# Kernel tuning notes

Hardware: AMD Instinct MI355X
Metric: run time of the kernel (lower is better)

The kernel has to match this reference:

```python
import jax, jax.numpy as jnp
import numpy as np

NUM_BLOCKS = 256
BLOCK_SIZE = 256
BATCH = 16
MAX_BLOCKS = 8            # max_context_len = MAX_BLOCKS * BLOCK_SIZE = 2048
NUM_HEADS = 32
NUM_KV_HEADS = 8
HEAD_DIM = 128
SCALE = 1.0 / np.sqrt(HEAD_DIM).astype(np.float32)


def setup_inputs() -> dict:
    key = jax.random.key(0)
    ks = jax.random.split(key, 5)
    q = jax.random.normal(ks[0], (BATCH, NUM_HEADS, HEAD_DIM), dtype=jnp.float32)
    k = jax.random.normal(ks[1], (BATCH, NUM_KV_HEADS, HEAD_DIM), dtype=jnp.float32)
    v = jax.random.normal(ks[2], (BATCH, NUM_KV_HEADS, HEAD_DIM), dtype=jnp.float32)
    k_cache = jax.random.normal(ks[3], (NUM_BLOCKS, BLOCK_SIZE, NUM_KV_HEADS, HEAD_DIM), dtype=jnp.float32)
    v_cache = jax.random.normal(ks[4], (NUM_BLOCKS, BLOCK_SIZE, NUM_KV_HEADS, HEAD_DIM), dtype=jnp.float32)
    rng = np.random.default_rng(0)
    # distinct blocks per sequence (16*8 = 128 <= 256 available blocks)
    block_tables = rng.permutation(NUM_BLOCKS)[: BATCH * MAX_BLOCKS].reshape(BATCH, MAX_BLOCKS).astype(np.int32)
    context_lens = rng.integers(1, MAX_BLOCKS * BLOCK_SIZE + 1, size=(BATCH,)).astype(np.int32)
    pos = context_lens - 1  # slot of the token being written this decode step
    slot_mapping = (block_tables[np.arange(BATCH), pos // BLOCK_SIZE] * BLOCK_SIZE + pos % BLOCK_SIZE).astype(np.int32)
    return {
        "q": q, "k": k, "v": v,
        "k_cache": k_cache, "v_cache": v_cache,
        "block_tables": jnp.asarray(block_tables),
        "context_lens": jnp.asarray(context_lens),
        "slot_mapping": jnp.asarray(slot_mapping),
    }


def _store_kv(key_t, value_t, kc_flat, vc_flat, slot_mapping):
    # scatter new K/V tokens to cache slots; slot < 0 means skip
    valid = slot_mapping >= 0
    safe = jnp.where(valid, slot_mapping, 0)
    kc_flat = kc_flat.at[safe].set(jnp.where(valid[:, None, None], key_t, kc_flat[safe]))
    vc_flat = vc_flat.at[safe].set(jnp.where(valid[:, None, None], value_t, vc_flat[safe]))
    return kc_flat, vc_flat


def reference(q, k, v, k_cache, v_cache, block_tables, context_lens, slot_mapping):
    # 1) store current-step K/V to paged cache (flattened view)
    kc_flat = k_cache.reshape(-1, NUM_KV_HEADS, HEAD_DIM)
    vc_flat = v_cache.reshape(-1, NUM_KV_HEADS, HEAD_DIM)
    kc_flat, vc_flat = _store_kv(k, v, kc_flat, vc_flat, slot_mapping)
    kc = kc_flat.reshape(NUM_BLOCKS, BLOCK_SIZE, NUM_KV_HEADS, HEAD_DIM)
    vc = vc_flat.reshape(NUM_BLOCKS, BLOCK_SIZE, NUM_KV_HEADS, HEAD_DIM)

    # 2) gather K/V blocks per sequence -> [B, L, KV, D], L = MAX_BLOCKS*BLOCK_SIZE
    safe_bt = jnp.clip(block_tables, 0, NUM_BLOCKS - 1)
    L = MAX_BLOCKS * BLOCK_SIZE
    k_g = kc[safe_bt.reshape(-1)].reshape(BATCH, L, NUM_KV_HEADS, HEAD_DIM)
    v_g = vc[safe_bt.reshape(-1)].reshape(BATCH, L, NUM_KV_HEADS, HEAD_DIM)
    kv_mask = jnp.arange(L)[None, :] < context_lens[:, None]  # [B, L]

    # 3) grouped-query attention, one query token per sequence
    G = NUM_HEADS // NUM_KV_HEADS
    q_g = q.reshape(BATCH, NUM_KV_HEADS, G, HEAD_DIM)
    scores = jnp.einsum('bkgd,blkd->bkgl', q_g, k_g) * SCALE  # [B, KV, G, L]
    scores = jnp.where(kv_mask[:, None, None, :], scores, -1e9)
    w = jax.nn.softmax(scores, axis=-1)
    out = jnp.einsum('bkgl,blkd->bkgd', w, v_g)
    return out.reshape(BATCH, NUM_HEADS, HEAD_DIM)
```

## Files before the change

kernel.cpp:

```cpp
#include <hip/hip_runtime.h>

#define BATCH 16
#define NUM_HEADS 32
#define NUM_KV 8
#define GQ 4
#define HD 128
#define PAGE 256
#define MAXB 8
#define NS 8
#define TPS 256
#define QSCALE 0.08838834764831845f

#define WS_STRIDE 520

__global__ __launch_bounds__(256) void pa_partial(
    const float* __restrict__ q,
    const float* __restrict__ knew,
    const float* __restrict__ vnew,
    const float* __restrict__ kc,
    const float* __restrict__ vc,
    const int* __restrict__ block_tables,
    const int* __restrict__ context_lens,
    float* __restrict__ ws)
{
  int blk = blockIdx.x;
  int t = blk >> 8;
  int r = blk & 255;
  int b = (t << 2) | (r & 3);
  int kvh = (r >> 2) & 7;
  int split = ((r >> 5) + (t << 1)) & 7;

  int ctx = context_lens[b];
  int start = split * TPS;
  if (start >= ctx) return;
  int n = min(TPS, ctx - start);
  int page = block_tables[b * MAXB + split];
  int pbase = page * PAGE;

  int tid = threadIdx.x;
  int w = tid >> 6;
  int lane = tid & 63;
  int grp = lane >> 4;
  int j = lane & 15;
  int tb = w * 4 + grp;

  __shared__ float4 s_pv[TPS];
  __shared__ float s_redM[4][GQ];
  __shared__ float s_redL[4][GQ];
  __shared__ float s_acc[4][GQ][HD];

  float qr[GQ][8];
  #pragma unroll
  for (int g = 0; g < GQ; ++g) {
    const float* qp = q + ((size_t)(b * NUM_HEADS + kvh * GQ + g)) * HD;
    float4 a = *(const float4*)(qp + j * 4);
    float4 c = *(const float4*)(qp + 64 + j * 4);
    qr[g][0]=a.x*QSCALE; qr[g][1]=a.y*QSCALE; qr[g][2]=a.z*QSCALE; qr[g][3]=a.w*QSCALE;
    qr[g][4]=c.x*QSCALE; qr[g][5]=c.y*QSCALE; qr[g][6]=c.z*QSCALE; qr[g][7]=c.w*QSCALE;
  }

  const float* knew_row = knew + (size_t)(b * NUM_KV + kvh) * HD + j * 4;
  const float* vnew_row = vnew + (size_t)(b * NUM_KV + kvh) * HD + j * 4;
  size_t base_off = ((size_t)pbase * NUM_KV + kvh) * HD + j * 4;
  const float* kbase = kc + base_off;
  const float* vbase = vc + base_off;
  int newpos = ctx - 1 - start;

  int iters = (n + 15) >> 4;

  #pragma unroll 2
  for (int i = 0; i < iters; ++i) {
    int tl = tb + i * 16;
    int tlc = (tl < n) ? tl : 0;
    const float* krow = (tlc == newpos) ? knew_row
                                        : kbase + (size_t)tlc * (NUM_KV * HD);
    float4 k0 = *(const float4*)(krow);
    float4 k1 = *(const float4*)(krow + 64);
    float kk[8] = {k0.x,k0.y,k0.z,k0.w,k1.x,k1.y,k1.z,k1.w};
    float s0 = 0.f, s1 = 0.f, s2 = 0.f, s3 = 0.f;
    #pragma unroll
    for (int e = 0; e < 8; ++e) {
      s0 += qr[0][e] * kk[e];
      s1 += qr[1][e] * kk[e];
      s2 += qr[2][e] * kk[e];
      s3 += qr[3][e] * kk[e];
    }
    #pragma unroll
    for (int mask = 1; mask <= 8; mask <<= 1) {
      s0 += __shfl_xor(s0, mask);
      s1 += __shfl_xor(s1, mask);
      s2 += __shfl_xor(s2, mask);
      s3 += __shfl_xor(s3, mask);
    }
    if (j < 4) {
      float val = (j == 0) ? s0 : (j == 1) ? s1 : (j == 2) ? s2 : s3;
      ((float*)&s_pv[tl])[j] = val;
    }
  }
  __syncthreads();

  float4 sc = s_pv[tid];
  bool valid = tid < n;
  float sv0 = valid ? sc.x : -1e30f;
  float sv1 = valid ? sc.y : -1e30f;
  float sv2 = valid ? sc.z : -1e30f;
  float sv3 = valid ? sc.w : -1e30f;
  float m0 = sv0, m1 = sv1, m2 = sv2, m3 = sv3;
  #pragma unroll
  for (int mask = 1; mask <= 32; mask <<= 1) {
    m0 = fmaxf(m0, __shfl_xor(m0, mask));
    m1 = fmaxf(m1, __shfl_xor(m1, mask));
    m2 = fmaxf(m2, __shfl_xor(m2, mask));
    m3 = fmaxf(m3, __shfl_xor(m3, mask));
  }
  if (lane == 0) {
    s_redM[w][0] = m0; s_redM[w][1] = m1; s_redM[w][2] = m2; s_redM[w][3] = m3;
  }
  __syncthreads();
  float Mg[GQ];
  #pragma unroll
  for (int g = 0; g < GQ; ++g)
    Mg[g] = fmaxf(fmaxf(s_redM[0][g], s_redM[1][g]), fmaxf(s_redM[2][g], s_redM[3][g]));
  float4 p4;
  p4.x = __expf(sv0 - Mg[0]);
  p4.y = __expf(sv1 - Mg[1]);
  p4.z = __expf(sv2 - Mg[2]);
  p4.w = __expf(sv3 - Mg[3]);
  s_pv[tid] = p4;
  float l0 = p4.x, l1 = p4.y, l2 = p4.z, l3 = p4.w;
  #pragma unroll
  for (int mask = 1; mask <= 32; mask <<= 1) {
    l0 += __shfl_xor(l0, mask);
    l1 += __shfl_xor(l1, mask);
    l2 += __shfl_xor(l2, mask);
    l3 += __shfl_xor(l3, mask);
  }
  if (lane == 0) {
    s_redL[w][0] = l0; s_redL[w][1] = l1; s_redL[w][2] = l2; s_redL[w][3] = l3;
  }
  __syncthreads();
  float Lg[GQ];
  #pragma unroll
  for (int g = 0; g < GQ; ++g)
    Lg[g] = s_redL[0][g] + s_redL[1][g] + s_redL[2][g] + s_redL[3][g];

  float acc[GQ][8];
  #pragma unroll
  for (int g = 0; g < GQ; ++g)
    #pragma unroll
    for (int e = 0; e < 8; ++e) acc[g][e] = 0.f;

  #pragma unroll 2
  for (int i = 0; i < iters; ++i) {
    int tl = tb + i * 16;
    int tlc = (tl < n) ? tl : 0;
    const float* vrow = (tlc == newpos) ? vnew_row
                                        : vbase + (size_t)tlc * (NUM_KV * HD);
    float4 v0 = *(const float4*)(vrow);
    float4 v1 = *(const float4*)(vrow + 64);
    float vv[8] = {v0.x,v0.y,v0.z,v0.w,v1.x,v1.y,v1.z,v1.w};
    float4 pp = s_pv[tl];
    #pragma unroll
    for (int e = 0; e < 8; ++e) {
      acc[0][e] += pp.x * vv[e];
      acc[1][e] += pp.y * vv[e];
      acc[2][e] += pp.z * vv[e];
      acc[3][e] += pp.w * vv[e];
    }
  }

  #pragma unroll
  for (int g = 0; g < GQ; ++g)
    #pragma unroll
    for (int e = 0; e < 8; ++e) {
      acc[g][e] += __shfl_xor(acc[g][e], 16);
      acc[g][e] += __shfl_xor(acc[g][e], 32);
    }
  if (lane < 16) {
    #pragma unroll
    for (int g = 0; g < GQ; ++g) {
      #pragma unroll
      for (int e = 0; e < 4; ++e) s_acc[w][g][j * 4 + e] = acc[g][e];
      #pragma unroll
      for (int e = 4; e < 8; ++e) s_acc[w][g][64 + j * 4 + e - 4] = acc[g][e];
    }
  }
  __syncthreads();

  float* outp = ws + (size_t)(((b * NUM_KV) + kvh) * NS + split) * WS_STRIDE;
  #pragma unroll
  for (int idx = tid; idx < GQ * HD; idx += 256) {
    int g = idx >> 7;
    int d = idx & 127;
    float A = s_acc[0][g][d] + s_acc[1][g][d] + s_acc[2][g][d] + s_acc[3][g][d];
    outp[8 + idx] = A;
    if (d == 0) {
      outp[g] = Mg[g];
      outp[GQ + g] = Lg[g];
    }
  }
}

__global__ __launch_bounds__(128) void pa_reduce(
    const float* __restrict__ ws,
    const int* __restrict__ context_lens,
    float* __restrict__ out)
{
  int blk = blockIdx.x;
  int g  = blk & 3;
  int kv = (blk >> 2) & 7;
  int b  = blk >> 5;
  int d  = threadIdx.x;
  int ctx = context_lens[b];
  int ns = (ctx + TPS - 1) / TPS;
  const float* base = ws + (size_t)((b * NUM_KV + kv) * NS) * WS_STRIDE;

  float M = -1e30f;
  for (int s = 0; s < ns; ++s) M = fmaxf(M, base[s * WS_STRIDE + g]);
  float Lsum = 0.f, A = 0.f;
  for (int s = 0; s < ns; ++s) {
    float e = __expf(base[s * WS_STRIDE + g] - M);
    Lsum += base[s * WS_STRIDE + GQ + g] * e;
    A    += base[s * WS_STRIDE + 8 + g * HD + d] * e;
  }
  out[((size_t)(b * NUM_HEADS) + kv * GQ + g) * HD + d] = A / Lsum;
}

extern "C" void kernel_launch(void* const* d_in, const int* in_sizes, int n_in,
                              void* d_out, int out_size, void* d_ws, size_t ws_size,
                              hipStream_t stream) {
  const float* q  = (const float*)d_in[0];
  const float* k  = (const float*)d_in[1];
  const float* v  = (const float*)d_in[2];
  const float* kc = (const float*)d_in[3];
  const float* vc = (const float*)d_in[4];
  const int* block_tables = (const int*)d_in[5];
  const int* context_lens = (const int*)d_in[6];

  float* ws = (float*)d_ws;
  float* out = (float*)d_out;

  pa_partial<<<BATCH * NUM_KV * NS, 256, 0, stream>>>(
      q, k, v, kc, vc, block_tables, context_lens, ws);
  pa_reduce<<<BATCH * NUM_KV * GQ, 128, 0, stream>>>(ws, context_lens, out);
}
```

Baseline: 39.59 us.

## Use persistent work-stealing blocks with finer 128-token splits for paged attention

Replaces the fixed one-block-per-(batch, kv head, split) grid with 1024 persistent blocks that claim work items through a global atomic counter, which is reset each call with a memset. When the workspace is large enough it halves the split size to 128 tokens (16 splits), giving finer load balancing across sequences of uneven context length. The cost is an extra memset launch, an atomic plus a barrier per item, and more partials for the reduce kernel to combine. With 128-token splits, half the threads sit idle in the softmax phase.

```diff
diff --git a/kernel.cpp b/kernel.cpp
--- a/kernel.cpp
+++ b/kernel.cpp
@@ -7,13 +7,14 @@
 #define HD 128
 #define PAGE 256
 #define MAXB 8
-#define NS 8
-#define TPS 256
+#define NGROUP (BATCH * NUM_KV)
 #define QSCALE 0.08838834764831845f
 
 #define WS_STRIDE 520
-
-__global__ __launch_bounds__(256) void pa_partial(
+#define PART_OFF 128
+
+template <int NSPLIT, int TPSZ>
+__global__ __launch_bounds__(256) void pa_partial_steal(
     const float* __restrict__ q,
     const float* __restrict__ knew,
     const float* __restrict__ vnew,
@@ -23,197 +24,223 @@
     const int* __restrict__ context_lens,
     float* __restrict__ ws)
 {
-  int blk = blockIdx.x;
-  int t = blk >> 8;
-  int r = blk & 255;
-  int b = (t << 2) | (r & 3);
-  int kvh = (r >> 2) & 7;
-  int split = ((r >> 5) + (t << 1)) & 7;
-
-  int ctx = context_lens[b];
-  int start = split * TPS;
-  if (start >= ctx) return;
-  int n = min(TPS, ctx - start);
-  int page = block_tables[b * MAXB + split];
-  int pbase = page * PAGE;
+  constexpr int NITEM = NGROUP * NSPLIT;
+  int* cnt = (int*)ws;
+  float* part = ws + PART_OFF;
 
   int tid = threadIdx.x;
   int w = tid >> 6;
   int lane = tid & 63;
-  int grp = lane >> 4;
+  int grp16 = lane >> 4;
   int j = lane & 15;
-  int tb = w * 4 + grp;
-
-  __shared__ float4 s_pv[TPS];
+  int tb = w * 4 + grp16;
+
+  __shared__ float4 s_pv[TPSZ];
   __shared__ float s_redM[4][GQ];
   __shared__ float s_redL[4][GQ];
   __shared__ float s_acc[4][GQ][HD];
-
-  float qr[GQ][8];
-  #pragma unroll
-  for (int g = 0; g < GQ; ++g) {
-    const float* qp = q + ((size_t)(b * NUM_HEADS + kvh * GQ + g)) * HD;
-    float4 a = *(const float4*)(qp + j * 4);
-    float4 c = *(const float4*)(qp + 64 + j * 4);
-    qr[g][0]=a.x*QSCALE; qr[g][1]=a.y*QSCALE; qr[g][2]=a.z*QSCALE; qr[g][3]=a.w*QSCALE;
-    qr[g][4]=c.x*QSCALE; qr[g][5]=c.y*QSCALE; qr[g][6]=c.z*QSCALE; qr[g][7]=c.w*QSCALE;
-  }
-
-  const float* knew_row = knew + (size_t)(b * NUM_KV + kvh) * HD + j * 4;
-  const float* vnew_row = vnew + (size_t)(b * NUM_KV + kvh) * HD + j * 4;
-  size_t base_off = ((size_t)pbase * NUM_KV + kvh) * HD + j * 4;
-  const float* kbase = kc + base_off;
-  const float* vbase = vc + base_off;
-  int newpos = ctx - 1 - start;
-
-  int iters = (n + 15) >> 4;
-
-  #pragma unroll 2
-  for (int i = 0; i < iters; ++i) {
-    int tl = tb + i * 16;
-    int tlc = (tl < n) ? tl : 0;
-    const float* krow = (tlc == newpos) ? knew_row
-                                        : kbase + (size_t)tlc * (NUM_KV * HD);
-    float4 k0 = *(const float4*)(krow);
-    float4 k1 = *(const float4*)(krow + 64);
-    float kk[8] = {k0.x,k0.y,k0.z,k0.w,k1.x,k1.y,k1.z,k1.w};
-    float s0 = 0.f, s1 = 0.f, s2 = 0.f, s3 = 0.f;
-    #pragma unroll
-    for (int e = 0; e < 8; ++e) {
-      s0 += qr[0][e] * kk[e];
-      s1 += qr[1][e] * kk[e];
-      s2 += qr[2][e] * kk[e];
-      s3 += qr[3][e] * kk[e];
-    }
-    #pragma unroll
-    for (int mask = 1; mask <= 8; mask <<= 1) {
-      s0 += __shfl_xor(s0, mask);
-      s1 += __shfl_xor(s1, mask);
-      s2 += __shfl_xor(s2, mask);
-      s3 += __shfl_xor(s3, mask);
-    }
-    if (j < 4) {
-      float val = (j == 0) ? s0 : (j == 1) ? s1 : (j == 2) ? s2 : s3;
-      ((float*)&s_pv[tl])[j] = val;
-    }
-  }
-  __syncthreads();
-
-  float4 sc = s_pv[tid];
-  bool valid = tid < n;
-  float sv0 = valid ? sc.x : -1e30f;
-  float sv1 = valid ? sc.y : -1e30f;
-  float sv2 = valid ? sc.z : -1e30f;
-  float sv3 = valid ? sc.w : -1e30f;
-  float m0 = sv0, m1 = sv1, m2 = sv2, m3 = sv3;
-  #pragma unroll
-  for (int mask = 1; mask <= 32; mask <<= 1) {
-    m0 = fmaxf(m0, __shfl_xor(m0, mask));
-    m1 = fmaxf(m1, __shfl_xor(m1, mask));
-    m2 = fmaxf(m2, __shfl_xor(m2, mask));
-    m3 = fmaxf(m3, __shfl_xor(m3, mask));
-  }
-  if (lane == 0) {
-    s_redM[w][0] = m0; s_redM[w][1] = m1; s_redM[w][2] = m2; s_redM[w][3] = m3;
-  }
-  __syncthreads();
-  float Mg[GQ];
-  #pragma unroll
-  for (int g = 0; g < GQ; ++g)
-    Mg[g] = fmaxf(fmaxf(s_redM[0][g], s_redM[1][g]), fmaxf(s_redM[2][g], s_redM[3][g]));
-  float4 p4;
-  p4.x = __expf(sv0 - Mg[0]);
-  p4.y = __expf(sv1 - Mg[1]);
-  p4.z = __expf(sv2 - Mg[2]);
-  p4.w = __expf(sv3 - Mg[3]);
-  s_pv[tid] = p4;
-  float l0 = p4.x, l1 = p4.y, l2 = p4.z, l3 = p4.w;
-  #pragma unroll
-  for (int mask = 1; mask <= 32; mask <<= 1) {
-    l0 += __shfl_xor(l0, mask);
-    l1 += __shfl_xor(l1, mask);
-    l2 += __shfl_xor(l2, mask);
-    l3 += __shfl_xor(l3, mask);
-  }
-  if (lane == 0) {
-    s_redL[w][0] = l0; s_redL[w][1] = l1; s_redL[w][2] = l2; s_redL[w][3] = l3;
-  }
-  __syncthreads();
-  float Lg[GQ];
-  #pragma unroll
-  for (int g = 0; g < GQ; ++g)
-    Lg[g] = s_redL[0][g] + s_redL[1][g] + s_redL[2][g] + s_redL[3][g];
-
-  float acc[GQ][8];
-  #pragma unroll
-  for (int g = 0; g < GQ; ++g)
-    #pragma unroll
-    for (int e = 0; e < 8; ++e) acc[g][e] = 0.f;
-
-  #pragma unroll 2
-  for (int i = 0; i < iters; ++i) {
-    int tl = tb + i * 16;
-    int tlc = (tl < n) ? tl : 0;
-    const float* vrow = (tlc == newpos) ? vnew_row
-                                        : vbase + (size_t)tlc * (NUM_KV * HD);
-    float4 v0 = *(const float4*)(vrow);
-    float4 v1 = *(const float4*)(vrow + 64);
-    float vv[8] = {v0.x,v0.y,v0.z,v0.w,v1.x,v1.y,v1.z,v1.w};
-    float4 pp = s_pv[tl];
-    #pragma unroll
-    for (int e = 0; e < 8; ++e) {
-      acc[0][e] += pp.x * vv[e];
-      acc[1][e] += pp.y * vv[e];
-      acc[2][e] += pp.z * vv[e];
-      acc[3][e] += pp.w * vv[e];
-    }
-  }
-
-  #pragma unroll
-  for (int g = 0; g < GQ; ++g)
-    #pragma unroll
-    for (int e = 0; e < 8; ++e) {
-      acc[g][e] += __shfl_xor(acc[g][e], 16);
-      acc[g][e] += __shfl_xor(acc[g][e], 32);
-    }
-  if (lane < 16) {
+  __shared__ int s_item;
+
+  for (;;) {
+    if (tid == 0) s_item = atomicAdd(cnt, 1);
+    __syncthreads();
+    int item = s_item;
+    if (item >= NITEM) return;
+
+    int kvh = item & 7;
+    int b = (item >> 3) & 15;
+    int split = item >> 7;
+    int ctx = context_lens[b];
+    int start = split * TPSZ;
+    if (start >= ctx) continue;
+    int n = min(TPSZ, ctx - start);
+    int page = block_tables[b * MAXB + (start >> 8)];
+    int pbase = page * PAGE + (start & (PAGE - 1));
+
+    float qr[GQ][8];
     #pragma unroll
     for (int g = 0; g < GQ; ++g) {
-      #pragma unroll
-      for (int e = 0; e < 4; ++e) s_acc[w][g][j * 4 + e] = acc[g][e];
-      #pragma unroll
-      for (int e = 4; e < 8; ++e) s_acc[w][g][64 + j * 4 + e - 4] = acc[g][e];
-    }
-  }
-  __syncthreads();
-
-  float* outp = ws + (size_t)(((b * NUM_KV) + kvh) * NS + split) * WS_STRIDE;
-  #pragma unroll
-  for (int idx = tid; idx < GQ * HD; idx += 256) {
-    int g = idx >> 7;
-    int d = idx & 127;
-    float A = s_acc[0][g][d] + s_acc[1][g][d] + s_acc[2][g][d] + s_acc[3][g][d];
-    outp[8 + idx] = A;
-    if (d == 0) {
-      outp[g] = Mg[g];
-      outp[GQ + g] = Lg[g];
+      const float* qp = q + ((size_t)(b * NUM_HEADS + kvh * GQ + g)) * HD;
+      float4 a = *(const float4*)(qp + j * 4);
+      float4 c = *(const float4*)(qp + 64 + j * 4);
+      qr[g][0]=a.x*QSCALE; qr[g][1]=a.y*QSCALE; qr[g][2]=a.z*QSCALE; qr[g][3]=a.w*QSCALE;
+      qr[g][4]=c.x*QSCALE; qr[g][5]=c.y*QSCALE; qr[g][6]=c.z*QSCALE; qr[g][7]=c.w*QSCALE;
+    }
+
+    const float* knew_row = knew + (size_t)(b * NUM_KV + kvh) * HD + j * 4;
+    const float* vnew_row = vnew + (size_t)(b * NUM_KV + kvh) * HD + j * 4;
+    size_t base_off = ((size_t)pbase * NUM_KV + kvh) * HD + j * 4;
+    const float* kbase = kc + base_off;
+    const float* vbase = vc + base_off;
+    int newpos = ctx - 1 - start;
+
+    int iters = (n + 15) >> 4;
+
+    #pragma unroll 2
+    for (int i = 0; i < iters; ++i) {
+      int tl = tb + i * 16;
+      int tlc = (tl < n) ? tl : 0;
+      const float* krow = (tlc == newpos) ? knew_row
+                                          : kbase + (size_t)tlc * (NUM_KV * HD);
+      float4 k0 = *(const float4*)(krow);
+      float4 k1 = *(const float4*)(krow + 64);
+      float kk[8] = {k0.x,k0.y,k0.z,k0.w,k1.x,k1.y,k1.z,k1.w};
+      float s0 = 0.f, s1 = 0.f, s2 = 0.f, s3 = 0.f;
+      #pragma unroll
+      for (int e = 0; e < 8; ++e) {
+        s0 += qr[0][e] * kk[e];
+        s1 += qr[1][e] * kk[e];
+        s2 += qr[2][e] * kk[e];
+        s3 += qr[3][e] * kk[e];
+      }
+      #pragma unroll
+      for (int mask = 1; mask <= 8; mask <<= 1) {
+        s0 += __shfl_xor(s0, mask);
+        s1 += __shfl_xor(s1, mask);
+        s2 += __shfl_xor(s2, mask);
+        s3 += __shfl_xor(s3, mask);
+      }
+      if (j < 4) {
+        float val = (j == 0) ? s0 : (j == 1) ? s1 : (j == 2) ? s2 : s3;
+        ((float*)&s_pv[tl])[j] = val;
+      }
+    }
+    __syncthreads();
+
+    constexpr int NWT = TPSZ / 64;
+    float Mg[GQ], Lg[GQ];
+    {
+      float4 sc;
+      float sv0, sv1, sv2, sv3;
+      if (tid < TPSZ) {
+        sc = s_pv[tid];
+        bool valid = tid < n;
+        sv0 = valid ? sc.x : -1e30f;
+        sv1 = valid ? sc.y : -1e30f;
+        sv2 = valid ? sc.z : -1e30f;
+        sv3 = valid ? sc.w : -1e30f;
+        float m0 = sv0, m1 = sv1, m2 = sv2, m3 = sv3;
+        #pragma unroll
+        for (int mask = 1; mask <= 32; mask <<= 1) {
+          m0 = fmaxf(m0, __shfl_xor(m0, mask));
+          m1 = fmaxf(m1, __shfl_xor(m1, mask));
+          m2 = fmaxf(m2, __shfl_xor(m2, mask));
+          m3 = fmaxf(m3, __shfl_xor(m3, mask));
+        }
+        if (lane == 0) {
+          s_redM[w][0] = m0; s_redM[w][1] = m1; s_redM[w][2] = m2; s_redM[w][3] = m3;
+        }
+      }
+      __syncthreads();
+      #pragma unroll
+      for (int g = 0; g < GQ; ++g) {
+        float mm = s_redM[0][g];
+        #pragma unroll
+        for (int ww = 1; ww < NWT; ++ww) mm = fmaxf(mm, s_redM[ww][g]);
+        Mg[g] = mm;
+      }
+      if (tid < TPSZ) {
+        float4 p4;
+        p4.x = __expf(sv0 - Mg[0]);
+        p4.y = __expf(sv1 - Mg[1]);
+        p4.z = __expf(sv2 - Mg[2]);
+        p4.w = __expf(sv3 - Mg[3]);
+        s_pv[tid] = p4;
+        float l0 = p4.x, l1 = p4.y, l2 = p4.z, l3 = p4.w;
+        #pragma unroll
+        for (int mask = 1; mask <= 32; mask <<= 1) {
+          l0 += __shfl_xor(l0, mask);
+          l1 += __shfl_xor(l1, mask);
+          l2 += __shfl_xor(l2, mask);
+          l3 += __shfl_xor(l3, mask);
+        }
+        if (lane == 0) {
+          s_redL[w][0] = l0; s_redL[w][1] = l1; s_redL[w][2] = l2; s_redL[w][3] = l3;
+        }
+      }
+      __syncthreads();
+      #pragma unroll
+      for (int g = 0; g < GQ; ++g) {
+        float ll = s_redL[0][g];
+        #pragma unroll
+        for (int ww = 1; ww < NWT; ++ww) ll += s_redL[ww][g];
+        Lg[g] = ll;
+      }
+    }
+
+    float acc[GQ][8];
+    #pragma unroll
+    for (int g = 0; g < GQ; ++g)
+      #pragma unroll
+      for (int e = 0; e < 8; ++e) acc[g][e] = 0.f;
+
+    #pragma unroll 2
+    for (int i = 0; i < iters; ++i) {
+      int tl = tb + i * 16;
+      int tlc = (tl < n) ? tl : 0;
+      const float* vrow = (tlc == newpos) ? vnew_row
+                                          : vbase + (size_t)tlc * (NUM_KV * HD);
+      float4 v0 = *(const float4*)(vrow);
+      float4 v1 = *(const float4*)(vrow + 64);
+      float vv[8] = {v0.x,v0.y,v0.z,v0.w,v1.x,v1.y,v1.z,v1.w};
+      float4 pp = s_pv[tl];
+      #pragma unroll
+      for (int e = 0; e < 8; ++e) {
+        acc[0][e] += pp.x * vv[e];
+        acc[1][e] += pp.y * vv[e];
+        acc[2][e] += pp.z * vv[e];
+        acc[3][e] += pp.w * vv[e];
+      }
+    }
+
+    #pragma unroll
+    for (int g = 0; g < GQ; ++g)
+      #pragma unroll
+      for (int e = 0; e < 8; ++e) {
+        acc[g][e] += __shfl_xor(acc[g][e], 16);
+        acc[g][e] += __shfl_xor(acc[g][e], 32);
+      }
+    if (lane < 16) {
+      #pragma unroll
+      for (int g = 0; g < GQ; ++g) {
+        #pragma unroll
+        for (int e = 0; e < 4; ++e) s_acc[w][g][j * 4 + e] = acc[g][e];
+        #pragma unroll
+        for (int e = 4; e < 8; ++e) s_acc[w][g][64 + j * 4 + e - 4] = acc[g][e];
+      }
+    }
+    __syncthreads();
+
+    float* outp = part + (size_t)(((b * NUM_KV) + kvh) * NSPLIT + split) * WS_STRIDE;
+    #pragma unroll
+    for (int idx = tid; idx < GQ * HD; idx += 256) {
+      int g = idx >> 7;
+      int d = idx & 127;
+      float A = s_acc[0][g][d] + s_acc[1][g][d] + s_acc[2][g][d] + s_acc[3][g][d];
+      outp[8 + idx] = A;
+      if (d == 0) {
+        outp[g] = Mg[g];
+        outp[GQ + g] = Lg[g];
+      }
     }
   }
 }
 
+template <int NSPLIT, int TPSZ>
 __global__ __launch_bounds__(128) void pa_reduce(
     const float* __restrict__ ws,
     const int* __restrict__ context_lens,
     float* __restrict__ out)
 {
+  const float* part = ws + PART_OFF;
   int blk = blockIdx.x;
   int g  = blk & 3;
   int kv = (blk >> 2) & 7;
   int b  = blk >> 5;
   int d  = threadIdx.x;
   int ctx = context_lens[b];
-  int ns = (ctx + TPS - 1) / TPS;
-  const float* base = ws + (size_t)((b * NUM_KV + kv) * NS) * WS_STRIDE;
+  int ns = (ctx + TPSZ - 1) / TPSZ;
+  const float* base = part + (size_t)((b * NUM_KV + kv) * NSPLIT) * WS_STRIDE;
 
   float M = -1e30f;
   for (int s = 0; s < ns; ++s) M = fmaxf(M, base[s * WS_STRIDE + g]);
@@ -240,7 +267,16 @@
   float* ws = (float*)d_ws;
   float* out = (float*)d_out;
 
-  pa_partial<<<BATCH * NUM_KV * NS, 256, 0, stream>>>(
-      q, k, v, kc, vc, block_tables, context_lens, ws);
-  pa_reduce<<<BATCH * NUM_KV * GQ, 128, 0, stream>>>(ws, context_lens, out);
+  hipMemsetAsync(d_ws, 0, 512, stream);
+
+  size_t need16 = 512 + (size_t)NGROUP * 16 * WS_STRIDE * sizeof(float);
+  if (ws_size >= need16) {
+    pa_partial_steal<16, 128><<<1024, 256, 0, stream>>>(
+        q, k, v, kc, vc, block_tables, context_lens, ws);
+    pa_reduce<16, 128><<<BATCH * NUM_KV * GQ, 128, 0, stream>>>(ws, context_lens, out);
+  } else {
+    pa_partial_steal<8, 256><<<1024, 256, 0, stream>>>(
+        q, k, v, kc, vc, block_tables, context_lens, ws);
+    pa_reduce<8, 256><<<BATCH * NUM_KV * GQ, 128, 0, stream>>>(ws, context_lens, out);
+  }
 }
```

Measured after the change: 70.03 us. 1.77x slower.

## Balance split-K work across blocks using device-computed adaptive partition size

Applied to the files above, without the earlier changes.

Replaces the fixed page-sized splits with a work-balanced partition: each block reads all context lengths, computes a target tokens-per-piece from the total, and maps its block index to a (sequence, kv head, piece) triple so pieces are roughly equal in size across sequences. Pieces may straddle two pages, so page lookup is done per token. This is meant to remove load imbalance where long sequences left some blocks doing full pages while many blocks exited early. It adds per-block prefix computation over all sequences, more workspace slots, and a possibly longer reduction loop.

```diff
diff --git a/kernel.cpp b/kernel.cpp
--- a/kernel.cpp
+++ b/kernel.cpp
@@ -7,12 +7,24 @@
 #define HD 128
 #define PAGE 256
 #define MAXB 8
-#define NS 8
-#define TPS 256
+#define NGROUP (BATCH * NUM_KV)
 #define QSCALE 0.08838834764831845f
 
 #define WS_STRIDE 520
-
+#define GRID 1280
+
+template <int SLOTS, int NT, int MINP>
+__device__ __forceinline__ int calc_P(const int* cx, int& total) {
+  total = 0;
+  #pragma unroll
+  for (int bb = 0; bb < BATCH; ++bb) total += cx[bb];
+  int P = (total * NUM_KV + NT - 1) / NT;
+  if (P < MINP) P = MINP;
+  if (P > 256) P = 256;
+  return P;
+}
+
+template <int SLOTS, int NT, int MINP>
 __global__ __launch_bounds__(256) void pa_partial(
     const float* __restrict__ q,
     const float* __restrict__ knew,
@@ -23,19 +35,33 @@
     const int* __restrict__ context_lens,
     float* __restrict__ ws)
 {
+  int cx[BATCH];
+  #pragma unroll
+  for (int bb = 0; bb < BATCH; ++bb) cx[bb] = context_lens[bb];
+  int total;
+  int P = calc_P<SLOTS, NT, MINP>(cx, total);
+
   int blk = blockIdx.x;
-  int t = blk >> 8;
-  int r = blk & 255;
-  int b = (t << 2) | (r & 3);
-  int kvh = (r >> 2) & 7;
-  int split = ((r >> 5) + (t << 1)) & 7;
-
-  int ctx = context_lens[b];
-  int start = split * TPS;
-  if (start >= ctx) return;
-  int n = min(TPS, ctx - start);
-  int page = block_tables[b * MAXB + split];
-  int pbase = page * PAGE;
+  int b = -1, local = 0, acc_ = 0;
+  #pragma unroll
+  for (int bb = 0; bb < BATCH; ++bb) {
+    int nb = (cx[bb] + P - 1) / P; if (nb > SLOTS) nb = SLOTS;
+    int np = nb * NUM_KV;
+    if (b < 0 && blk < acc_ + np) { b = bb; local = blk - acc_; }
+    acc_ += np;
+  }
+  if (b < 0) return;
+  int ctx = cx[b];
+  int nb = (ctx + P - 1) / P; if (nb > SLOTS) nb = SLOTS;
+  int sz = (ctx + nb - 1) / nb;
+  int kvh = local & 7;
+  int piece = local >> 3;
+  int start = piece * sz;
+  int n = min(sz, ctx - start);
+
+  int pg0 = block_tables[b * MAXB + (start >> 8)];
+  int pg1 = block_tables[b * MAXB + ((start + n - 1) >> 8)];
+  int seg0 = start >> 8;
 
   int tid = threadIdx.x;
   int w = tid >> 6;
@@ -44,7 +70,7 @@
   int j = lane & 15;
   int tb = w * 4 + grp;
 
-  __shared__ float4 s_pv[TPS];
+  __shared__ float4 s_pv[256];
   __shared__ float s_redM[4][GQ];
   __shared__ float s_redL[4][GQ];
   __shared__ float s_acc[4][GQ][HD];
@@ -61,9 +87,7 @@
 
   const float* knew_row = knew + (size_t)(b * NUM_KV + kvh) * HD + j * 4;
   const float* vnew_row = vnew + (size_t)(b * NUM_KV + kvh) * HD + j * 4;
-  size_t base_off = ((size_t)pbase * NUM_KV + kvh) * HD + j * 4;
-  const float* kbase = kc + base_off;
-  const float* vbase = vc + base_off;
+  size_t lane_off = (size_t)kvh * HD + j * 4;
   int newpos = ctx - 1 - start;
 
   int iters = (n + 15) >> 4;
@@ -72,8 +96,11 @@
   for (int i = 0; i < iters; ++i) {
     int tl = tb + i * 16;
     int tlc = (tl < n) ? tl : 0;
+    int tok = start + tlc;
+    int pg = ((tok >> 8) == seg0) ? pg0 : pg1;
+    int row = pg * PAGE + (tok & 255);
     const float* krow = (tlc == newpos) ? knew_row
-                                        : kbase + (size_t)tlc * (NUM_KV * HD);
+                                        : kc + (size_t)row * (NUM_KV * HD) + lane_off;
     float4 k0 = *(const float4*)(krow);
     float4 k1 = *(const float4*)(krow + 64);
     float kk[8] = {k0.x,k0.y,k0.z,k0.w,k1.x,k1.y,k1.z,k1.w};
@@ -154,8 +181,11 @@
   for (int i = 0; i < iters; ++i) {
     int tl = tb + i * 16;
     int tlc = (tl < n) ? tl : 0;
+    int tok = start + tlc;
+    int pg = ((tok >> 8) == seg0) ? pg0 : pg1;
+    int row = pg * PAGE + (tok & 255);
     const float* vrow = (tlc == newpos) ? vnew_row
-                                        : vbase + (size_t)tlc * (NUM_KV * HD);
+                                        : vc + (size_t)row * (NUM_KV * HD) + lane_off;
     float4 v0 = *(const float4*)(vrow);
     float4 v1 = *(const float4*)(vrow + 64);
     float vv[8] = {v0.x,v0.y,v0.z,v0.w,v1.x,v1.y,v1.z,v1.w};
@@ -187,7 +217,7 @@
   }
   __syncthreads();
 
-  float* outp = ws + (size_t)(((b * NUM_KV) + kvh) * NS + split) * WS_STRIDE;
+  float* outp = ws + (size_t)(((b * NUM_KV) + kvh) * SLOTS + piece) * WS_STRIDE;
   #pragma unroll
   for (int idx = tid; idx < GQ * HD; idx += 256) {
     int g = idx >> 7;
@@ -201,24 +231,31 @@
   }
 }
 
+template <int SLOTS, int NT, int MINP>
 __global__ __launch_bounds__(128) void pa_reduce(
     const float* __restrict__ ws,
     const int* __restrict__ context_lens,
     float* __restrict__ out)
 {
+  int cx[BATCH];
+  #pragma unroll
+  for (int bb = 0; bb < BATCH; ++bb) cx[bb] = context_lens[bb];
+  int total;
+  int P = calc_P<SLOTS, NT, MINP>(cx, total);
+
   int blk = blockIdx.x;
   int g  = blk & 3;
   int kv = (blk >> 2) & 7;
   int b  = blk >> 5;
   int d  = threadIdx.x;
-  int ctx = context_lens[b];
-  int ns = (ctx + TPS - 1) / TPS;
-  const float* base = ws + (size_t)((b * NUM_KV + kv) * NS) * WS_STRIDE;
+  int ctx = cx[b];
+  int nb = (ctx + P - 1) / P; if (nb > SLOTS) nb = SLOTS;
+  const float* base = ws + (size_t)((b * NUM_KV + kv) * SLOTS) * WS_STRIDE;
 
   float M = -1e30f;
-  for (int s = 0; s < ns; ++s) M = fmaxf(M, base[s * WS_STRIDE + g]);
+  for (int s = 0; s < nb; ++s) M = fmaxf(M, base[s * WS_STRIDE + g]);
   float Lsum = 0.f, A = 0.f;
-  for (int s = 0; s < ns; ++s) {
+  for (int s = 0; s < nb; ++s) {
     float e = __expf(base[s * WS_STRIDE + g] - M);
     Lsum += base[s * WS_STRIDE + GQ + g] * e;
     A    += base[s * WS_STRIDE + 8 + g * HD + d] * e;
@@ -240,7 +277,14 @@
   float* ws = (float*)d_ws;
   float* out = (float*)d_out;
 
-  pa_partial<<<BATCH * NUM_KV * NS, 256, 0, stream>>>(
-      q, k, v, kc, vc, block_tables, context_lens, ws);
-  pa_reduce<<<BATCH * NUM_KV * GQ, 128, 0, stream>>>(ws, context_lens, out);
-}
+  size_t need32 = (size_t)NGROUP * 32 * WS_STRIDE * sizeof(float);
+  if (ws_size >= need32) {
+    pa_partial<32, 768, 64><<<GRID, 256, 0, stream>>>(
+        q, k, v, kc, vc, block_tables, context_lens, ws);
+    pa_reduce<32, 768, 64><<<BATCH * NUM_KV * GQ, 128, 0, stream>>>(ws, context_lens, out);
+  } else {
+    pa_partial<8, 512, 256><<<GRID, 256, 0, stream>>>(
+        q, k, v, kc, vc, block_tables, context_lens, ws);
+    pa_reduce<8, 512, 256><<<BATCH * NUM_KV * GQ, 128, 0, stream>>>(ws, context_lens, out);
+  }
+}
```

New measurement: 40.40 us. 1.02x slower.
